# Performance work log

Hardware: AMD Instinct MI355X
Metric: run time of the kernel (lower is better)

## Reference

```python
import jax, jax.numpy as jnp
import numpy as np

SIG_EPS = 0.1
IN_DIM = 256
OUT_DIM = 64


def setup_inputs() -> dict:
    key = jax.random.key(0)
    ks = jax.random.split(key, 6)
    B, S, Q = 32, 512, 512
    return {
        "phi_support": jax.random.normal(ks[0], (B, S, IN_DIM), jnp.float32),
        "y_support": jax.random.normal(ks[1], (B, S, OUT_DIM), jnp.float32),
        "phi_query": jax.random.normal(ks[2], (B, Q, IN_DIM), jnp.float32),
        "y_query": jax.random.normal(ks[3], (B, Q, OUT_DIM), jnp.float32),
        # learned parameters (K init'd to zeros in torch, use small randn for a non-trivial test)
        "K": jax.random.normal(ks[4], (IN_DIM, OUT_DIM), jnp.float32) * 0.02,
        "L_asym": jax.random.normal(ks[5], (IN_DIM, IN_DIM), jnp.float32) * 0.1,
    }


def reference(phi_support, y_support, phi_query, y_query, K, L_asym):
    sig_eps = jnp.float32(SIG_EPS)
    log_sig_eps = jnp.log(sig_eps)
    out_dim = K.shape[1]

    L = L_asym @ L_asym.T  # [I, I]
    # nobs > 0 branch (n_support = 512)
    posterior_L = jnp.einsum('bsi,bsj->bij', phi_support, phi_support) + L[None]  # [B,I,I]
    posterior_L_inv = jnp.linalg.inv(posterior_L)
    rhs = jnp.einsum('bsi,bso->bio', phi_support, y_support) + (L @ K)[None]  # [B,I,O]
    posterior_K = posterior_L_inv @ rhs  # [B,I,O]

    mu_pred = phi_query @ posterior_K  # [B,Q,O]
    # spread_fac = 1 + diag quadratic form phi Linv phi^T  -> [B,Q]
    spread_fac = 1.0 + jnp.einsum('bqi,bij,bqj->bq', phi_query, posterior_L_inv, phi_query)
    eye_eps = jnp.eye(out_dim, dtype=phi_query.dtype) * sig_eps
    sig_pred = spread_fac[..., None, None] * eye_eps  # [B,Q,O,O]

    # predictive_nll: inverse of sig_pred is an exactly scaled identity, so the
    # quadratic form y^T inv(sig_pred) y == ||y||^2 / (spread_fac * sig_eps) (same math)
    diff = y_query - mu_pred
    quadf = jnp.sum(diff * diff, axis=-1) / (spread_fac * sig_eps)  # [B,Q]
    logdet = out_dim * (jnp.log(spread_fac) + log_sig_eps)  # [B,Q]
    predictive_nll = logdet.mean() + quadf.mean()

    return (mu_pred, sig_pred, predictive_nll)
```

## Files before the change

### kernel.cpp

```cpp
#include <hip/hip_runtime.h>
#include <math.h>

#define B 32
#define S 512
#define Q 512
#define I 256
#define O 64
#define SIG_EPS 0.1f
#define LOG_SIG_EPS (-2.3025850929940457f)

#define WS_L 0
#define WS_T1 (WS_L + 65536)
#define WS_LK (WS_T1 + 16384)
#define WS_M (WS_LK + 16384)
#define WS_RHS (WS_M + B * 65536)
#define WS_D (WS_RHS + B * 16384)
#define WS_PK (WS_D + 2 * B * 4096)
#define WS_SP (WS_PK + B * 16384)
#define WS_NLL (WS_SP + B * 512)

#define OUT_MU_ELEMS (B * Q * O)
#define OUT_SIG_ELEMS (B * Q * O * O)
#define OUT_NLL_IDX (OUT_MU_ELEMS + OUT_SIG_ELEMS)

__device__ __forceinline__ void fma4x4(const float4 av, const float4 bv, float acc[4][4]) {
  const float ar[4] = {av.x, av.y, av.z, av.w};
  const float br[4] = {bv.x, bv.y, bv.z, bv.w};
#pragma unroll
  for (int i = 0; i < 4; ++i)
#pragma unroll
    for (int j = 0; j < 4; ++j) acc[i][j] += ar[i] * br[j];
}

__device__ __forceinline__ void load_direct64(float* dst, int ds, const float* src, int ss, int t) {
#pragma unroll
  for (int m = 0; m < 4; ++m) {
    int r = (t >> 4) + 16 * m, c4 = (t & 15) * 4;
    *(float4*)&dst[r * ds + c4] = *(const float4*)&src[(size_t)r * ss + c4];
  }
}
__device__ __forceinline__ void load_trans64(float* dst, int ds , const float* src, int ss, int t) {
#pragma unroll
  for (int m = 0; m < 4; ++m) {
    int r = (t >> 4) + 16 * m, c4 = (t & 15) * 4;
    float4 v = *(const float4*)&src[(size_t)r * ss + c4];
    dst[(c4 + 0) * ds + r] = v.x;
    dst[(c4 + 1) * ds + r] = v.y;
    dst[(c4 + 2) * ds + r] = v.z;
    dst[(c4 + 3) * ds + r] = v.w;
  }
}
template <int SA, int SB>
__device__ __forceinline__ void gemm64(const float* At, const float* Bs, int tr, int tc, float acc[4][4]) {
#pragma unroll 8
  for (int kk = 0; kk < 64; ++kk) {
    float4 a = *(const float4*)&At[kk * SA + tr * 4];
    float4 b = *(const float4*)&Bs[kk * SB + tc * 4];
    fma4x4(a, b, acc);
  }
}

#define SC4(V) \
  V.x *= pivinv; V.y *= pivinv; V.z *= pivinv; V.w *= pivinv
#define UP4(V, R) \
  V.x -= g * R.x; V.y -= g * R.y; V.z -= g * R.z; V.w -= g * R.w

template <int TS>
__device__ void gj64(const float* T, float* rowbuf, float* Dout, int t) {
  int r = t >> 2, q = t & 3;
  int lane = t & 63;
  float4 A0 = *(const float4*)&T[r * TS + q * 16 + 0];
  float4 A1 = *(const float4*)&T[r * TS + q * 16 + 4];
  float4 A2 = *(const float4*)&T[r * TS + q * 16 + 8];
  float4 A3 = *(const float4*)&T[r * TS + q * 16 + 12];
#define IC(c) (((q * 16 + (c)) == r) ? 1.f : 0.f)
  float4 I0 = make_float4(IC(0), IC(1), IC(2), IC(3));
  float4 I1 = make_float4(IC(4), IC(5), IC(6), IC(7));
  float4 I2 = make_float4(IC(8), IC(9), IC(10), IC(11));
  float4 I3 = make_float4(IC(12), IC(13), IC(14), IC(15));
#undef IC
  for (int p = 0; p < 64; ++p) {
    float* RA = rowbuf + (p & 1) * 128;
    float* RI = RA + 64;
    if (r == p) {
      ((float4*)&RA[q * 16])[0] = A0; ((float4*)&RA[q * 16])[1] = A1;
      ((float4*)&RA[q * 16])[2] = A2; ((float4*)&RA[q * 16])[3] = A3;
      ((float4*)&RI[q * 16])[0] = I0; ((float4*)&RI[q * 16])[1] = I1;
      ((float4*)&RI[q * 16])[2] = I2; ((float4*)&RI[q * 16])[3] = I3;
    }
    __syncthreads();
    float pivinv = 1.0f / RA[p];
    int s = p & 15;
    float4 blk = (s < 8) ? ((s < 4) ? A0 : A1) : ((s < 12) ? A2 : A3);
    int sc = s & 3;
    float ap = (sc == 0) ? blk.x : (sc == 1) ? blk.y : (sc == 2) ? blk.z : blk.w;
    float f = __shfl(ap, (lane & ~3) | (p >> 4), 64);
    float4 ra0 = ((const float4*)&RA[q * 16])[0], ra1 = ((const float4*)&RA[q * 16])[1];
    float4 ra2 = ((const float4*)&RA[q * 16])[2], ra3 = ((const float4*)&RA[q * 16])[3];
    float4 ri0 = ((const float4*)&RI[q * 16])[0], ri1 = ((const float4*)&RI[q * 16])[1];
    float4 ri2 = ((const float4*)&RI[q * 16])[2], ri3 = ((const float4*)&RI[q * 16])[3];
    if (r == p) {
      SC4(A0); SC4(A1); SC4(A2); SC4(A3);
      SC4(I0); SC4(I1); SC4(I2); SC4(I3);
    } else {
      float g = f * pivinv;
      UP4(A0, ra0); UP4(A1, ra1); UP4(A2, ra2); UP4(A3, ra3);
      UP4(I0, ri0); UP4(I1, ri1); UP4(I2, ri2); UP4(I3, ri3);
    }
  }
  ((float4*)&Dout[r * 64 + q * 16])[0] = I0;
  ((float4*)&Dout[r * 64 + q * 16])[1] = I1;
  ((float4*)&Dout[r * 64 + q * 16])[2] = I2;
  ((float4*)&Dout[r * 64 + q * 16])[3] = I3;
}

__global__ __launch_bounds__(256) void k_pre1(const float* __restrict__ La, const float* __restrict__ Km,
                                              float* __restrict__ Lm, float* __restrict__ T1,
                                              float* __restrict__ spread, float* __restrict__ nllacc) {
  __shared__ float sA[16 * 68];
  __shared__ float sB[16 * 68];
  int blk = blockIdx.x, t = threadIdx.x;
  if (blk >= 20) {
    int idx = (blk - 20) * 256 + t;
    spread[idx] = 1.0f;
    if (idx == 0) nllacc[0] = 0.f;
    return;
  }
  int tr = t >> 4, tc = t & 15;
  float acc[4][4] = {};
  if (blk < 16) {
    int i0 = (blk >> 2) * 64, j0 = (blk & 3) * 64;
    for (int ks = 0; ks < 256; ks += 16) {
      __syncthreads();
#pragma unroll
      for (int m = 0; m < 4; ++m) {
        int r = (t >> 4) + 16 * m, kk = t & 15;
        sA[kk * 68 + r] = La[(size_t)(i0 + r) * 256 + ks + kk];
        sB[kk * 68 + r] = La[(size_t)(j0 + r) * 256 + ks + kk];
      }
      __syncthreads();
#pragma unroll
      for (int kk = 0; kk < 16; ++kk) {
        float4 a = *(const float4*)&sA[kk * 68 + tr * 4];
        float4 bv = *(const float4*)&sB[kk * 68 + tc * 4];
        fma4x4(a, bv, acc);
      }
    }
#pragma unroll
    for (int mi = 0; mi < 4; ++mi) {
      float4 v = {acc[mi][0], acc[mi][1], acc[mi][2], acc[mi][3]};
      *(float4*)&Lm[(size_t)(i0 + tr * 4 + mi) * 256 + j0 + tc * 4] = v;
    }
  } else {
    int i0 = (blk - 16) * 64;
    for (int ks = 0; ks < 256; ks += 16) {
      __syncthreads();
#pragma unroll
      for (int m = 0; m < 4; ++m) {
        int kk = (t >> 6) + 4 * m, c = t & 63;
        sA[kk * 68 + c] = La[(size_t)(ks + kk) * 256 + i0 + c];
        sB[kk * 68 + c] = Km[(size_t)(ks + kk) * 64 + c];
      }
      __syncthreads();
#pragma unroll
      for (int kk = 0; kk < 16; ++kk) {
        float4 a = *(const float4*)&sA[kk * 68 + tr * 4];
        float4 bv = *(const float4*)&sB[kk * 68 + tc * 4];
        fma4x4(a, bv, acc);
      }
    }
#pragma unroll
    for (int mi = 0; mi < 4; ++mi) {
      float4 v = {acc[mi][0], acc[mi][1], acc[mi][2], acc[mi][3]};
      *(float4*)&T1[(size_t)(i0 + tr * 4 + mi) * 64 + tc * 4] = v;
    }
  }
}

__global__ __launch_bounds__(256) void k_gram(const float* __restrict__ phi_s, const float* __restrict__ y_s,
                                              const float* __restrict__ Lm, const float* __restrict__ La,
                                              const float* __restrict__ T1, float* __restrict__ M,
                                              float* __restrict__ RHS, float* __restrict__ LK,
                                              float* __restrict__ Dbuf) {
  __shared__ float Ps[16][64];
  __shared__ float Ws[16][64];
  __shared__ float trbuf[64 * 68];
  __shared__ float rowbuf[256];
  int b = blockIdx.x, y = blockIdx.y;
  int t = threadIdx.x;
  int tr = t >> 4, tc = t & 15;
  float acc[4][4] = {};

  if (y == 14) {
    if (b >= 4) return;
    int i0 = b * 64;
    for (int ks = 0; ks < 256; ks += 16) {
      __syncthreads();
#pragma unroll
      for (int m = 0; m < 4; ++m) {
        trbuf[(t & 15) * 68 + (t >> 4) + 16 * m] = La[(size_t)(i0 + (t >> 4) + 16 * m) * 256 + ks + (t & 15)];
        Ws[(t >> 6) + 4 * m][t & 63] = T1[(size_t)(ks + (t >> 6) + 4 * m) * 64 + (t & 63)];
      }
      __syncthreads();
#pragma unroll
      for (int kk = 0; kk < 16; ++kk) {
        float4 a = *(const float4*)&trbuf[kk * 68 + tr * 4];
        float4 bv = *(const float4*)&Ws[kk][tc * 4];
        fma4x4(a, bv, acc);
      }
    }
#pragma unroll
    for (int mi = 0; mi < 4; ++mi) {
      float4 v = {acc[mi][0], acc[mi][1], acc[mi][2], acc[mi][3]};
      *(float4*)&LK[(size_t)(i0 + tr * 4 + mi) * 64 + tc * 4] = v;
    }
    return;
  }

  const int TI[10] = {0, 0, 0, 0, 1, 1, 1, 2, 2, 3};
  const int TJ[10] = {0, 1, 2, 3, 1, 2, 3, 2, 3, 3};
  bool isRHS = (y >= 10);
  int it = isRHS ? (y - 10) : TI[y];
  int jt = isRHS ? 0 : TJ[y];
  int i0 = it * 64, j0 = jt * 64;
  const float* Pb = phi_s + (size_t)b * S * I;
  const float* Wb = isRHS ? (y_s + (size_t)b * S * O) : Pb;
  int wstride = isRHS ? O : I;
  int wcol = isRHS ? 0 : j0;
  int lr = t >> 6, lc = t & 63;
  for (int ks = 0; ks < S; ks += 16) {
    __syncthreads();
#pragma unroll
    for (int m = 0; m < 4; ++m) {
      Ps[lr + 4 * m][lc] = Pb[(size_t)(ks + lr + 4 * m) * I + i0 + lc];
      Ws[lr + 4 * m][lc] = Wb[(size_t)(ks + lr + 4 * m) * wstride + wcol + lc];
    }
    __syncthreads();
#pragma unroll
    for (int kk = 0; kk < 16; ++kk) {
      float4 a = *(const float4*)&Ps[kk][tr * 4];
      float4 bv = *(const float4*)&Ws[kk][tc * 4];
      fma4x4(a, bv, acc);
    }
  }
  float* Mb = M + (size_t)b * 65536;
  if (!isRHS) {
#pragma unroll
    for (int mi = 0; mi < 4; ++mi) {
      int i = i0 + tr * 4 + mi;
      float4 add = *(const float4*)&Lm[(size_t)i * 256 + j0 + tc * 4];
      acc[mi][0] += add.x; acc[mi][1] += add.y; acc[mi][2] += add.z; acc[mi][3] += add.w;
      float4 v = {acc[mi][0], acc[mi][1], acc[mi][2], acc[mi][3]};
      *(float4*)&Mb[(size_t)i * 256 + j0 + tc * 4] = v;
    }
    if (it != jt) {
      __syncthreads();
#pragma unroll
      for (int mi = 0; mi < 4; ++mi)
#pragma unroll
        for (int cj = 0; cj < 4; ++cj) trbuf[(tc * 4 + cj) * 68 + tr * 4 + mi] = acc[mi][cj];
      __syncthreads();
#pragma unroll
      for (int m = 0; m < 4; ++m) {
        int rr = (t >> 4) + 16 * m, cc4 = (t & 15) * 4;
        float4 v = *(const float4*)&trbuf[rr * 68 + cc4];
        *(float4*)&Mb[(size_t)(j0 + rr) * 256 + i0 + cc4] = v;
      }
    } else if (it == 0) {
      __syncthreads();
#pragma unroll
      for (int mi = 0; mi < 4; ++mi) {
        float4 v = {acc[mi][0], acc[mi][1], acc[mi][2], acc[mi][3]};
        *(float4*)&trbuf[(tr * 4 + mi) * 68 + tc * 4] = v;
      }
      __syncthreads();
      gj64<68>(trbuf, rowbuf, Dbuf + (size_t)b * 4096, t);
    }
  } else {
#pragma unroll
    for (int mi = 0; mi < 4; ++mi) {
      float4 v = {acc[mi][0], acc[mi][1], acc[mi][2], acc[mi][3]};
      *(float4*)&RHS[(size_t)b * 16384 + (size_t)(i0 + tr * 4 + mi) * 64 + tc * 4] = v;
    }
  }
}

__global__ __launch_bounds__(256) void k_step(float* __restrict__ M, float* __restrict__ Dbuf, int kb) {
  __shared__ float shA[64 * 68];
  __shared__ float shB[64 * 64];
  __shared__ float shC[64 * 64];
  __shared__ float shD[64 * 68];
  __shared__ float rowbuf[256];
  int b = blockIdx.x, u = blockIdx.y;
  int i = u >> 2, j = u & 3;
  int t = threadIdx.x;
  int tr = t >> 4, tc = t & 15;
  float* Mb = M + (size_t)b * 65536;
  const float* Din = Dbuf + (size_t)(kb & 1) * (B * 4096) + (size_t)b * 4096;
  float* Dout = Dbuf + (size_t)((kb + 1) & 1) * (B * 4096) + (size_t)b * 4096;
  bool ik = (i == kb), jk = (j == kb);
  if (ik && jk) {
#pragma unroll
    for (int m = 0; m < 4; ++m) {
      int r = (t >> 4) + 16 * m, c4 = (t & 15) * 4;
      *(float4*)&Mb[(size_t)(kb * 64 + r) * 256 + kb * 64 + c4] = *(const float4*)&Din[r * 64 + c4];
    }
    return;
  }
  float acc[4][4] = {};
  if (ik) {
    load_trans64(shA, 68, Din, 64, t);
    load_direct64(shB, 64, &Mb[(size_t)(kb * 64) * 256 + j * 64], 256, t);
    __syncthreads();
    gemm64<68, 64>(shA, shB, tr, tc, acc);
#pragma unroll
    for (int mi = 0; mi < 4; ++mi) {
      float4 v = {acc[mi][0], acc[mi][1], acc[mi][2], acc[mi][3]};
      *(float4*)&Mb[(size_t)(kb * 64 + tr * 4 + mi) * 256 + j * 64 + tc * 4] = v;
    }
    return;
  }
  if (jk) {
    load_trans64(shA, 68, &Mb[(size_t)(i * 64) * 256 + kb * 64], 256, t);
    load_direct64(shB, 64, Din, 64, t);
    __syncthreads();
    gemm64<68, 64>(shA, shB, tr, tc, acc);
#pragma unroll
    for (int mi = 0; mi < 4; ++mi) {
      float4 v = {-acc[mi][0], -acc[mi][1], -acc[mi][2], -acc[mi][3]};
      *(float4*)&Mb[(size_t)(i * 64 + tr * 4 + mi) * 256 + kb * 64 + tc * 4] = v;
    }
    return;
  }
  load_trans64(shA, 68, Din, 64, t);
  load_direct64(shB, 64, &Mb[(size_t)(kb * 64) * 256 + j * 64], 256, t);
  load_trans64(shD, 68, &Mb[(size_t)(i * 64) * 256 + kb * 64], 256, t);
  __syncthreads();
  gemm64<68, 64>(shA, shB, tr, tc, acc);
#pragma unroll
  for (int mi = 0; mi < 4; ++mi) {
    float4 v = {acc[mi][0], acc[mi][1], acc[mi][2], acc[mi][3]};
    *(float4*)&shC[(tr * 4 + mi) * 64 + tc * 4] = v;
  }
  __syncthreads();
  float acc2[4][4] = {};
  gemm64<68, 64>(shD, shC, tr, tc, acc2);
  bool la = (kb < 3) && (i == kb + 1) && (j == kb + 1);
#pragma unroll
  for (int mi = 0; mi < 4; ++mi) {
    size_t off = (size_t)(i * 64 + tr * 4 + mi) * 256 + j * 64 + tc * 4;
    float4 old = *(const float4*)&Mb[off];
    float4 v = {old.x - acc2[mi][0], old.y - acc2[mi][1], old.z - acc2[mi][2], old.w - acc2[mi][3]};
    *(float4*)&Mb[off] = v;
    if (la) *(float4*)&shB[(tr * 4 + mi) * 64 + tc * 4] = v;
  }
  if (la) {
    __syncthreads();
    gj64<64>(shB, rowbuf, Dout, t);
  }
}

__global__ __launch_bounds__(256) void k_postK(const float* __restrict__ Minv, const float* __restrict__ RHS,
                                               const float* __restrict__ LK, float* __restrict__ PK) {
  int b = blockIdx.x, it = blockIdx.y;
  int i0 = it * 64;
  const float* A = Minv + (size_t)b * 65536;
  const float* G = RHS + (size_t)b * 16384;
  __shared__ float At[16][68];
  __shared__ float Bs[16][64];
  float acc[4][4] = {};
  int t = threadIdx.x, tr = t >> 4, tc = t & 15;
  int ar = t >> 2, ac4 = (t & 3) * 4;
  int br = t >> 6, bc = t & 63;
  for (int ks = 0; ks < 256; ks += 16) {
    __syncthreads();
    float4 av = *(const float4*)&A[(size_t)(i0 + ar) * 256 + ks + ac4];
    At[ac4 + 0][ar] = av.x; At[ac4 + 1][ar] = av.y; At[ac4 + 2][ar] = av.z; At[ac4 + 3][ar] = av.w;
#pragma unroll
    for (int m = 0; m < 4; ++m) {
      int kk = ks + br + 4 * m;
      Bs[br + 4 * m][bc] = G[(size_t)kk * 64 + bc] + LK[(size_t)kk * 64 + bc];
    }
    __syncthreads();
#pragma unroll
    for (int kk = 0; kk < 16; ++kk) {
      float4 a4 = *(const float4*)&At[kk][tr * 4];
      float4 b4 = *(const float4*)&Bs[kk][tc * 4];
      fma4x4(a4, b4, acc);
    }
  }
#pragma unroll
  for (int mi = 0; mi < 4; ++mi) {
    float4 v = {acc[mi][0], acc[mi][1], acc[mi][2], acc[mi][3]};
    *(float4*)&PK[(size_t)b * 16384 + (size_t)(i0 + tr * 4 + mi) * 64 + tc * 4] = v;
  }
}

__global__ __launch_bounds__(256) void k_muspread(const float* __restrict__ phi_q, const float* __restrict__ Minv,
                                                  const float* __restrict__ PK, float* __restrict__ mu,
                                                  float* __restrict__ spread) {
  int b = blockIdx.x, it = blockIdx.y, z = blockIdx.z;
  const float* A = phi_q + (size_t)b * Q * I;
  __shared__ float At[16][68];
  __shared__ float Bs[16][64];
  float acc[4][4] = {};
  int t = threadIdx.x, tr = t >> 4, tc = t & 15;
  int ar = t >> 2, ac4 = (t & 3) * 4;
  int br = t >> 6, bc = t & 63;
  int q0 = it * 64;
  if (z == 4) {
    const float* Bm = PK + (size_t)b * 16384;
    for (int ks = 0; ks < 256; ks += 16) {
      __syncthreads();
      float4 av = *(const float4*)&A[(size_t)(q0 + ar) * 256 + ks + ac4];
      At[ac4 + 0][ar] = av.x; At[ac4 + 1][ar] = av.y; At[ac4 + 2][ar] = av.z; At[ac4 + 3][ar] = av.w;
#pragma unroll
      for (int m = 0; m < 4; ++m) Bs[br + 4 * m][bc] = Bm[(size_t)(ks + br + 4 * m) * 64 + bc];
      __syncthreads();
#pragma unroll
      for (int kk = 0; kk < 16; ++kk) {
        float4 a4 = *(const float4*)&At[kk][tr * 4];
        float4 b4 = *(const float4*)&Bs[kk][tc * 4];
        fma4x4(a4, b4, acc);
      }
    }
#pragma unroll
    for (int mi = 0; mi < 4; ++mi) {
      float4 v = {acc[mi][0], acc[mi][1], acc[mi][2], acc[mi][3]};
      *(float4*)&mu[(size_t)b * Q * O + (size_t)(q0 + tr * 4 + mi) * 64 + tc * 4] = v;
    }
  } else {
    int j0 = z * 64;
    const float* Bm = Minv + (size_t)b * 65536;
    for (int ks = 0; ks < 256; ks += 16) {
      __syncthreads();
      float4 av = *(const float4*)&A[(size_t)(q0 + ar) * 256 + ks + ac4];
      At[ac4 + 0][ar] = av.x; At[ac4 + 1][ar] = av.y; At[ac4 + 2][ar] = av.z; At[ac4 + 3][ar] = av.w;
#pragma unroll
      for (int m = 0; m < 4; ++m) Bs[br + 4 * m][bc] = Bm[(size_t)(ks + br + 4 * m) * 256 + j0 + bc];
      __syncthreads();
#pragma unroll
      for (int kk = 0; kk < 16; ++kk) {
        float4 a4 = *(const float4*)&At[kk][tr * 4];
        float4 b4 = *(const float4*)&Bs[kk][tc * 4];
        fma4x4(a4, b4, acc);
      }
    }
    float rs[4];
#pragma unroll
    for (int mi = 0; mi < 4; ++mi) {
      int qrow = q0 + tr * 4 + mi;
      float4 pv = *(const float4*)&A[(size_t)qrow * 256 + j0 + tc * 4];
      rs[mi] = acc[mi][0] * pv.x + acc[mi][1] * pv.y + acc[mi][2] * pv.z + acc[mi][3] * pv.w;
    }
#pragma unroll
    for (int off = 1; off < 16; off <<= 1) {
#pragma unroll
      for (int mi = 0; mi < 4; ++mi) rs[mi] += __shfl_xor(rs[mi], off);
    }
    if (tc == 0) {
#pragma unroll
      for (int mi = 0; mi < 4; ++mi) atomicAdd(&spread[(size_t)b * Q + q0 + tr * 4 + mi], rs[mi]);
    }
  }
}

__global__ __launch_bounds__(256) void k_signll(const float* __restrict__ spread, float4* __restrict__ sig,
                                                const float* __restrict__ yq, const float* __restrict__ mu,
                                                float* __restrict__ nllacc) {
  int t = threadIdx.x;
  if (blockIdx.x < 65536) {
    size_t idx = (size_t)blockIdx.x * 256 + t;
    int p4 = (int)(idx & 15);
    int o = (int)((idx >> 4) & 63);
    size_t bq = idx >> 10;
    float sv = spread[bq] * SIG_EPS;
    float4 v;
    v.x = (p4 * 4 + 0 == o) ? sv : 0.f;
    v.y = (p4 * 4 + 1 == o) ? sv : 0.f;
    v.z = (p4 * 4 + 2 == o) ? sv : 0.f;
    v.w = (p4 * 4 + 3 == o) ? sv : 0.f;
    sig[idx] = v;
  } else {
    int bq = (blockIdx.x - 65536) * 256 + t;
    float sp = spread[bq];
    const float4* yv = (const float4*)(yq + (size_t)bq * 64);
    const float4* mv = (const float4*)(mu + (size_t)bq * 64);
    float ssd = 0.f;
#pragma unroll
    for (int i = 0; i < 16; ++i) {
      float4 a = yv[i], b = mv[i];
      float dx = a.x - b.x, dy = a.y - b.y, dz = a.z - b.z, dw = a.w - b.w;
      ssd += dx * dx + dy * dy + dz * dz + dw * dw;
    }
    float quadf = ssd / (sp * SIG_EPS);
    float ld = 64.0f * (logf(sp) + LOG_SIG_EPS);
    float val = (ld + quadf) * (1.0f / 16384.0f);
#pragma unroll
    for (int off = 32; off; off >>= 1) val += __shfl_down(val, off);
    if ((t & 63) == 0) atomicAdd(nllacc, val);
  }
}

__global__ void k_fin(const float* __restrict__ nllacc, float* __restrict__ out) {
  if (threadIdx.x == 0 && blockIdx.x == 0) out[0] = nllacc[0];
}

extern "C" void kernel_launch(void* const* d_in, const int* in_sizes, int n_in, void* d_out, int out_size,
                              void* d_ws, size_t ws_size, hipStream_t stream) {
  const float* phi_s = (const float*)d_in[0];
  const float* y_s = (const float*)d_in[1];
  const float* phi_q = (const float*)d_in[2];
  const float* y_q = (const float*)d_in[3];
  const float* Km = (const float*)d_in[4];
  const float* La = (const float*)d_in[5];

  float* ws = (float*)d_ws;
  float* Lm = ws + WS_L;
  float* T1 = ws + WS_T1;
  float* LKm = ws + WS_LK;
  float* Mbuf = ws + WS_M;
  float* RHSb = ws + WS_RHS;
  float* Dbuf = ws + WS_D;
  float* PKb = ws + WS_PK;
  float* spread = ws + WS_SP;
  float* nllacc = ws + WS_NLL;

  float* out_mu = (float*)d_out;
  float* out_sig = out_mu + OUT_MU_ELEMS;
  float* out_nll = out_mu + OUT_NLL_IDX;

  k_pre1<<<84, 256, 0, stream>>>(La, Km, Lm, T1, spread, nllacc);
  k_gram<<<dim3(B, 15), 256, 0, stream>>>(phi_s, y_s, Lm, La, T1, Mbuf, RHSb, LKm, Dbuf);
  for (int kb = 0; kb < 4; ++kb) k_step<<<dim3(B, 16), 256, 0, stream>>>(Mbuf, Dbuf, kb);
  k_postK<<<dim3(B, 4), 256, 0, stream>>>(Mbuf, RHSb, LKm, PKb);
  k_muspread<<<dim3(B, 8, 5), 256, 0, stream>>>(phi_q, Mbuf, PKb, out_mu, spread);
  k_signll<<<65600, 256, 0, stream>>>(spread, (float4*)out_sig, y_q, out_mu, nllacc);
  k_fin<<<1, 64, 0, stream>>>(nllacc, out_nll);
}
```

Before: 330.1 us.

## Move gram, posterior-K and mu/spread GEMMs to split-bf16 MFMA

Adds a conversion pass that writes phi_support and y_support as transposed hi/lo bf16 pairs. The Gram, RHS, posterior-K and mu/spread GEMMs now run on bf16 MFMA using three products (hh, hl, lh) to approximate fp32 accuracy. The blocked inversion now ping-pongs between two M buffers, and its final step emits the inverse directly as bf16 hi/lo. The spread atomics are replaced by a single direct write per query. The goal is to replace scalar fp32 FMA loops with matrix-core throughput, at the cost of extra conversion traffic, a larger workspace and a small precision risk. The 64M-element sig_pred write, which likely dominates, is unchanged.

```diff
diff --git a/kernel.cpp b/kernel.cpp
--- a/kernel.cpp
+++ b/kernel.cpp
@@ -10,19 +10,65 @@
 #define LOG_SIG_EPS (-2.3025850929940457f)
 
 #define WS_L 0
-#define WS_T1 (WS_L + 65536)
-#define WS_LK (WS_T1 + 16384)
-#define WS_M (WS_LK + 16384)
-#define WS_RHS (WS_M + B * 65536)
-#define WS_D (WS_RHS + B * 16384)
-#define WS_PK (WS_D + 2 * B * 4096)
-#define WS_SP (WS_PK + B * 16384)
-#define WS_NLL (WS_SP + B * 512)
+#define WS_T1 65536
+#define WS_LKT 81920
+#define WS_M0 98304
+#define WS_M1 2195456
+#define WS_RHST 4292608
+#define WS_D 4816896
+#define WS_SP 5079040
+#define WS_NLL 5095424
+#define WS_U16 5095488
+#define U_PTH 0
+#define U_PTL 4194304
+#define U_YTH 8388608
+#define U_YTL 9437184
+#define U_IVH 10485760
+#define U_IVL 12582912
+#define U_PKH 14680064
+#define U_PKL 15204352
 
 #define OUT_MU_ELEMS (B * Q * O)
 #define OUT_SIG_ELEMS (B * Q * O * O)
 #define OUT_NLL_IDX (OUT_MU_ELEMS + OUT_SIG_ELEMS)
 
+typedef short short8 __attribute__((ext_vector_type(8)));
+typedef float f32x4 __attribute__((ext_vector_type(4)));
+#define MFMA16(a, b, c) __builtin_amdgcn_mfma_f32_16x16x32_bf16(a, b, c, 0, 0, 0)
+
+__device__ __forceinline__ f32x4 mfma3(short8 ah, short8 al, short8 bh, short8 bl, f32x4 c) {
+  c = MFMA16(ah, bh, c);
+  c = MFMA16(ah, bl, c);
+  c = MFMA16(al, bh, c);
+  return c;
+}
+
+__device__ __forceinline__ unsigned short f2bf(float x) {
+  unsigned int u = __float_as_uint(x);
+  return (unsigned short)((u + 0x7fffu + ((u >> 16) & 1u)) >> 16);
+}
+__device__ __forceinline__ float bf2f(unsigned short h) { return __uint_as_float(((unsigned int)h) << 16); }
+__device__ __forceinline__ void split2(float x, unsigned short& h, unsigned short& l) {
+  h = f2bf(x);
+  l = f2bf(x - bf2f(h));
+}
+__device__ __forceinline__ void split4(float4 v, uint2& H, uint2& L) {
+  unsigned short h0, h1, h2, h3, l0, l1, l2, l3;
+  split2(v.x, h0, l0); split2(v.y, h1, l1); split2(v.z, h2, l2); split2(v.w, h3, l3);
+  H.x = (unsigned)h0 | ((unsigned)h1 << 16); H.y = (unsigned)h2 | ((unsigned)h3 << 16);
+  L.x = (unsigned)l0 | ((unsigned)l1 << 16); L.y = (unsigned)l2 | ((unsigned)l3 << 16);
+}
+__device__ __forceinline__ void cvt8(const float* p, short8& h8, short8& l8) {
+  float4 a = *(const float4*)p;
+  float4 b = *(const float4*)(p + 4);
+  uint2 H0, L0, H1, L1;
+  split4(a, H0, L0); split4(b, H1, L1);
+  union { uint2 q[2]; short8 s; } uh, ul;
+  uh.q[0] = H0; uh.q[1] = H1; ul.q[0] = L0; ul.q[1] = L1;
+  h8 = uh.s; l8 = ul.s;
+}
+__device__ __forceinline__ short8 ld8(const unsigned short* p) { return *(const short8*)(const void*)p; }
+
 __device__ __forceinline__ void fma4x4(const float4 av, const float4 bv, float acc[4][4]) {
   const float ar[4] = {av.x, av.y, av.z, av.w};
   const float br[4] = {bv.x, bv.y, bv.z, bv.w};
@@ -39,7 +85,7 @@
     *(float4*)&dst[r * ds + c4] = *(const float4*)&src[(size_t)r * ss + c4];
   }
 }
-__device__ __forceinline__ void load_trans64(float* dst, int ds , const float* src, int ss, int t) {
+__device__ __forceinline__ void load_trans64(float* dst, int ds, const float* src, int ss, int t) {
 #pragma unroll
   for (int m = 0; m < 4; ++m) {
     int r = (t >> 4) + 16 * m, c4 = (t & 15) * 4;
@@ -60,10 +106,8 @@
   }
 }
 
-#define SC4(V) \
-  V.x *= pivinv; V.y *= pivinv; V.z *= pivinv; V.w *= pivinv
-#define UP4(V, R) \
-  V.x -= g * R.x; V.y -= g * R.y; V.z -= g * R.z; V.w -= g * R.w
+#define SC4(V) V.x *= pivinv; V.y *= pivinv; V.z *= pivinv; V.w *= pivinv
+#define UP4(V, R) V.x -= g * R.x; V.y -= g * R.y; V.z -= g * R.z; V.w -= g * R.w
 
 template <int TS>
 __device__ void gj64(const float* T, float* rowbuf, float* Dout, int t) {
@@ -114,18 +158,60 @@
   ((float4*)&Dout[r * 64 + q * 16])[3] = I3;
 }
 
+__global__ __launch_bounds__(256) void k_cvt(const float* __restrict__ phi_s, const float* __restrict__ y_s,
+                                             unsigned short* __restrict__ PTh, unsigned short* __restrict__ PTl,
+                                             unsigned short* __restrict__ YTh, unsigned short* __restrict__ YTl,
+                                             float* __restrict__ nllacc) {
+  __shared__ unsigned short Hs[64][68];
+  __shared__ unsigned short Lo[64][68];
+  int blk = blockIdx.x, t = threadIdx.x;
+  if (blk == 0 && t == 0) nllacc[0] = 0.f;
+  const float* src;
+  unsigned short *dh, *dl;
+  int sstride;
+  if (blk < 1024) {
+    int b = blk >> 5, r = blk & 31, ic = r >> 3, sc = r & 7;
+    src = phi_s + ((size_t)b * 512 + sc * 64) * 256 + ic * 64;
+    sstride = 256;
+    size_t d0 = ((size_t)b * 256 + ic * 64) * 512 + sc * 64;
+    dh = PTh + d0; dl = PTl + d0;
+  } else {
+    int qq = blk - 1024, b = qq >> 3, sc = qq & 7;
+    src = y_s + ((size_t)b * 512 + sc * 64) * 64;
+    sstride = 64;
+    size_t d0 = ((size_t)b * 64) * 512 + sc * 64;
+    dh = YTh + d0; dl = YTl + d0;
+  }
+  int c = t & 63, rb = (t >> 6) * 16;
+#pragma unroll
+  for (int m = 0; m < 16; ++m) {
+    int s = rb + m;
+    float x = src[(size_t)s * sstride + c];
+    unsigned short h, l;
+    split2(x, h, l);
+    Hs[c][s] = h;
+    Lo[c][s] = l;
+  }
+  __syncthreads();
+  int il0 = t >> 4, c4 = (t & 15) * 4;
+#pragma unroll
+  for (int m = 0; m < 4; ++m) {
+    int il = il0 + 16 * m;
+    uint2 H, L;
+    H.x = (unsigned)Hs[il][c4] | ((unsigned)Hs[il][c4 + 1] << 16);
+    H.y = (unsigned)Hs[il][c4 + 2] | ((unsigned)Hs[il][c4 + 3] << 16);
+    L.x = (unsigned)Lo[il][c4] | ((unsigned)Lo[il][c4 + 1] << 16);
+    L.y = (unsigned)Lo[il][c4 + 2] | ((unsigned)Lo[il][c4 + 3] << 16);
+    *(uint2*)&dh[(size_t)il * 512 + c4] = H;
+    *(uint2*)&dl[(size_t)il * 512 + c4] = L;
+  }
+}
+
 __global__ __launch_bounds__(256) void k_pre1(const float* __restrict__ La, const float* __restrict__ Km,
-                                              float* __restrict__ Lm, float* __restrict__ T1,
-                                              float* __restrict__ spread, float* __restrict__ nllacc) {
+                                              float* __restrict__ Lm, float* __restrict__ T1) {
   __shared__ float sA[16 * 68];
   __shared__ float sB[16 * 68];
   int blk = blockIdx.x, t = threadIdx.x;
-  if (blk >= 20) {
-    int idx = (blk - 20) * 256 + t;
-    spread[idx] = 1.0f;
-    if (idx == 0) nllacc[0] = 0.f;
-    return;
-  }
   int tr = t >> 4, tc = t & 15;
   float acc[4][4] = {};
   if (blk < 16) {
@@ -177,115 +263,132 @@
   }
 }
 
-__global__ __launch_bounds__(256) void k_gram(const float* __restrict__ phi_s, const float* __restrict__ y_s,
-                                              const float* __restrict__ Lm, const float* __restrict__ La,
-                                              const float* __restrict__ T1, float* __restrict__ M,
-                                              float* __restrict__ RHS, float* __restrict__ LK,
-                                              float* __restrict__ Dbuf) {
-  __shared__ float Ps[16][64];
-  __shared__ float Ws[16][64];
+__global__ __launch_bounds__(256) void k_gram(
+    const unsigned short* __restrict__ PTh, const unsigned short* __restrict__ PTl,
+    const unsigned short* __restrict__ YTh, const unsigned short* __restrict__ YTl,
+    const float* __restrict__ Lm, const float* __restrict__ La, const float* __restrict__ T1,
+    float* __restrict__ M0, float* __restrict__ RHST, float* __restrict__ LKT, float* __restrict__ Dbuf) {
   __shared__ float trbuf[64 * 68];
   __shared__ float rowbuf[256];
-  int b = blockIdx.x, y = blockIdx.y;
-  int t = threadIdx.x;
-  int tr = t >> 4, tc = t & 15;
-  float acc[4][4] = {};
+  __shared__ float Ws[16 * 64];
+  int b = blockIdx.x, y = blockIdx.y, t = threadIdx.x;
 
   if (y == 14) {
     if (b >= 4) return;
     int i0 = b * 64;
+    int tr = t >> 4, tc = t & 15;
+    float acc[4][4] = {};
     for (int ks = 0; ks < 256; ks += 16) {
       __syncthreads();
 #pragma unroll
       for (int m = 0; m < 4; ++m) {
         trbuf[(t & 15) * 68 + (t >> 4) + 16 * m] = La[(size_t)(i0 + (t >> 4) + 16 * m) * 256 + ks + (t & 15)];
-        Ws[(t >> 6) + 4 * m][t & 63] = T1[(size_t)(ks + (t >> 6) + 4 * m) * 64 + (t & 63)];
+        Ws[((t >> 6) + 4 * m) * 64 + (t & 63)] = T1[(size_t)(ks + (t >> 6) + 4 * m) * 64 + (t & 63)];
       }
       __syncthreads();
 #pragma unroll
       for (int kk = 0; kk < 16; ++kk) {
         float4 a = *(const float4*)&trbuf[kk * 68 + tr * 4];
-        float4 bv = *(const float4*)&Ws[kk][tc * 4];
+        float4 bv = *(const float4*)&Ws[kk * 64 + tc * 4];
         fma4x4(a, bv, acc);
       }
     }
-#pragma unroll
-    for (int mi = 0; mi < 4; ++mi) {
-      float4 v = {acc[mi][0], acc[mi][1], acc[mi][2], acc[mi][3]};
-      *(float4*)&LK[(size_t)(i0 + tr * 4 + mi) * 64 + tc * 4] = v;
+    __syncthreads();
+#pragma unroll
+    for (int mi = 0; mi < 4; ++mi)
+#pragma unroll
+      for (int cj = 0; cj < 4; ++cj) trbuf[(tr * 4 + mi) * 68 + tc * 4 + cj] = acc[mi][cj];
+    __syncthreads();
+    int rr0 = t >> 4, cc4 = (t & 15) * 4;
+#pragma unroll
+    for (int m = 0; m < 4; ++m) {
+      int rr = rr0 + 16 * m;
+      float4 v = {trbuf[(cc4 + 0) * 68 + rr], trbuf[(cc4 + 1) * 68 + rr], trbuf[(cc4 + 2) * 68 + rr],
+                  trbuf[(cc4 + 3) * 68 + rr]};
+      *(float4*)&LKT[(size_t)rr * 256 + i0 + cc4] = v;
     }
     return;
   }
 
-  const int TI[10] = {0, 0, 0, 0, 1, 1, 1, 2, 2, 3};
-  const int TJ[10] = {0, 1, 2, 3, 1, 2, 3, 2, 3, 3};
-  bool isRHS = (y >= 10);
-  int it = isRHS ? (y - 10) : TI[y];
-  int jt = isRHS ? 0 : TJ[y];
-  int i0 = it * 64, j0 = jt * 64;
-  const float* Pb = phi_s + (size_t)b * S * I;
-  const float* Wb = isRHS ? (y_s + (size_t)b * S * O) : Pb;
-  int wstride = isRHS ? O : I;
-  int wcol = isRHS ? 0 : j0;
-  int lr = t >> 6, lc = t & 63;
-  for (int ks = 0; ks < S; ks += 16) {
-    __syncthreads();
+  const int TIa[14] = {0, 0, 0, 0, 1, 1, 1, 2, 2, 3, 0, 1, 2, 3};
+  const int TJa[14] = {0, 1, 2, 3, 1, 2, 3, 2, 3, 3, 0, 0, 0, 0};
+  bool isR = (y >= 10);
+  int it = TIa[y], jt = TJa[y];
+  int i0 = it * 64, j0 = isR ? 0 : jt * 64;
+  int lane = t & 63, w = t >> 6, wr = w >> 1, wc = w & 1;
+  const unsigned short* Ah = PTh + (size_t)b * 256 * 512;
+  const unsigned short* Al = PTl + (size_t)b * 256 * 512;
+  const unsigned short* Bh = isR ? (YTh + (size_t)b * 64 * 512) : Ah;
+  const unsigned short* Bl = isR ? (YTl + (size_t)b * 64 * 512) : Al;
+  int ra0 = i0 + wr * 32 + (lane & 15);
+  int rb0 = j0 + wc * 32 + (lane & 15);
+  int klane = (lane >> 4) * 8;
+  f32x4 acc[2][2] = {};
+  for (int ks = 0; ks < 512; ks += 32) {
+    int kk = ks + klane;
+    short8 a0h = ld8(Ah + (size_t)ra0 * 512 + kk);
+    short8 a1h = ld8(Ah + (size_t)(ra0 + 16) * 512 + kk);
+    short8 a0l = ld8(Al + (size_t)ra0 * 512 + kk);
+    short8 a1l = ld8(Al + (size_t)(ra0 + 16) * 512 + kk);
+    short8 b0h = ld8(Bh + (size_t)rb0 * 512 + kk);
+    short8 b1h = ld8(Bh + (size_t)(rb0 + 16) * 512 + kk);
+    short8 b0l = ld8(Bl + (size_t)rb0 * 512 + kk);
+    short8 b1l = ld8(Bl + (size_t)(rb0 + 16) * 512 + kk);
+    acc[0][0] = mfma3(a0h, a0l, b0h, b0l, acc[0][0]);
+    acc[0][1] = mfma3(a0h, a0l, b1h, b1l, acc[0][1]);
+    acc[1][0] = mfma3(a1h, a1l, b0h, b0l, acc[1][0]);
+    acc[1][1] = mfma3(a1h, a1l, b1h, b1l, acc[1][1]);
+  }
+#pragma unroll
+  for (int ti = 0; ti < 2; ++ti)
+#pragma unroll
+    for (int tj = 0; tj < 2; ++tj)
+#pragma unroll
+      for (int r = 0; r < 4; ++r)
+        trbuf[(wr * 32 + ti * 16 + (lane >> 4) * 4 + r) * 68 + wc * 32 + tj * 16 + (lane & 15)] = acc[ti][tj][r];
+  __syncthreads();
+  int rr0 = t >> 4, cc4 = (t & 15) * 4;
+  if (!isR) {
+    float* Mb = M0 + (size_t)b * 65536;
+    bool d00 = (it == 0 && jt == 0);
 #pragma unroll
     for (int m = 0; m < 4; ++m) {
-      Ps[lr + 4 * m][lc] = Pb[(size_t)(ks + lr + 4 * m) * I + i0 + lc];
-      Ws[lr + 4 * m][lc] = Wb[(size_t)(ks + lr + 4 * m) * wstride + wcol + lc];
-    }
-    __syncthreads();
-#pragma unroll
-    for (int kk = 0; kk < 16; ++kk) {
-      float4 a = *(const float4*)&Ps[kk][tr * 4];
-      float4 bv = *(const float4*)&Ws[kk][tc * 4];
-      fma4x4(a, bv, acc);
-    }
-  }
-  float* Mb = M + (size_t)b * 65536;
-  if (!isRHS) {
-#pragma unroll
-    for (int mi = 0; mi < 4; ++mi) {
-      int i = i0 + tr * 4 + mi;
-      float4 add = *(const float4*)&Lm[(size_t)i * 256 + j0 + tc * 4];
-      acc[mi][0] += add.x; acc[mi][1] += add.y; acc[mi][2] += add.z; acc[mi][3] += add.w;
-      float4 v = {acc[mi][0], acc[mi][1], acc[mi][2], acc[mi][3]};
-      *(float4*)&Mb[(size_t)i * 256 + j0 + tc * 4] = v;
+      int rr = rr0 + 16 * m;
+      float4 v = *(float4*)&trbuf[rr * 68 + cc4];
+      float4 lv = *(const float4*)&Lm[(size_t)(i0 + rr) * 256 + j0 + cc4];
+      v.x += lv.x; v.y += lv.y; v.z += lv.z; v.w += lv.w;
+      *(float4*)&Mb[(size_t)(i0 + rr) * 256 + j0 + cc4] = v;
+      if (d00) *(float4*)&trbuf[rr * 68 + cc4] = v;
     }
     if (it != jt) {
-      __syncthreads();
-#pragma unroll
-      for (int mi = 0; mi < 4; ++mi)
-#pragma unroll
-        for (int cj = 0; cj < 4; ++cj) trbuf[(tc * 4 + cj) * 68 + tr * 4 + mi] = acc[mi][cj];
-      __syncthreads();
 #pragma unroll
       for (int m = 0; m < 4; ++m) {
-        int rr = (t >> 4) + 16 * m, cc4 = (t & 15) * 4;
-        float4 v = *(const float4*)&trbuf[rr * 68 + cc4];
+        int rr = rr0 + 16 * m;
+        float4 v = {trbuf[(cc4 + 0) * 68 + rr], trbuf[(cc4 + 1) * 68 + rr], trbuf[(cc4 + 2) * 68 + rr],
+                    trbuf[(cc4 + 3) * 68 + rr]};
+        float4 lv = *(const float4*)&Lm[(size_t)(j0 + rr) * 256 + i0 + cc4];
+        v.x += lv.x; v.y += lv.y; v.z += lv.z; v.w += lv.w;
         *(float4*)&Mb[(size_t)(j0 + rr) * 256 + i0 + cc4] = v;
       }
-    } else if (it == 0) {
-      __syncthreads();
-#pragma unroll
-      for (int mi = 0; mi < 4; ++mi) {
-        float4 v = {acc[mi][0], acc[mi][1], acc[mi][2], acc[mi][3]};
-        *(float4*)&trbuf[(tr * 4 + mi) * 68 + tc * 4] = v;
-      }
+    }
+    if (d00) {
       __syncthreads();
       gj64<68>(trbuf, rowbuf, Dbuf + (size_t)b * 4096, t);
     }
   } else {
 #pragma unroll
-    for (int mi = 0; mi < 4; ++mi) {
-      float4 v = {acc[mi][0], acc[mi][1], acc[mi][2], acc[mi][3]};
-      *(float4*)&RHS[(size_t)b * 16384 + (size_t)(i0 + tr * 4 + mi) * 64 + tc * 4] = v;
-    }
-  }
-}
-
-__global__ __launch_bounds__(256) void k_step(float* __restrict__ M, float* __restrict__ Dbuf, int kb) {
+    for (int m = 0; m < 4; ++m) {
+      int rr = rr0 + 16 * m;
+      float4 v = {trbuf[(cc4 + 0) * 68 + rr], trbuf[(cc4 + 1) * 68 + rr], trbuf[(cc4 + 2) * 68 + rr],
+                  trbuf[(cc4 + 3) * 68 + rr]};
+      *(float4*)&RHST[((size_t)b * 64 + rr) * 256 + i0 + cc4] = v;
+    }
+  }
+}
+
+__global__ __launch_bounds__(256) void k_step(const float* __restrict__ Msrc_, float* __restrict__ Mdst_,
+                                              float* __restrict__ Dbuf, unsigned short* __restrict__ IVh,
+                                              unsigned short* __restrict__ IVl, int kb) {
   __shared__ float shA[64 * 68];
   __shared__ float shB[64 * 64];
   __shared__ float shC[64 * 64];
@@ -295,46 +398,60 @@
   int i = u >> 2, j = u & 3;
   int t = threadIdx.x;
   int tr = t >> 4, tc = t & 15;
-  float* Mb = M + (size_t)b * 65536;
+  const float* Ms = Msrc_ + (size_t)b * 65536;
+  float* Md = Mdst_ + (size_t)b * 65536;
   const float* Din = Dbuf + (size_t)(kb & 1) * (B * 4096) + (size_t)b * 4096;
   float* Dout = Dbuf + (size_t)((kb + 1) & 1) * (B * 4096) + (size_t)b * 4096;
+  bool last = (kb == 3);
+  unsigned short* Yh = IVh + (size_t)b * 65536;
+  unsigned short* Yl = IVl + (size_t)b * 65536;
+  auto STORE = [&](int row, int col, float4 v) {
+    if (last) {
+      uint2 H, L;
+      split4(v, H, L);
+      *(uint2*)&Yh[(size_t)row * 256 + col] = H;
+      *(uint2*)&Yl[(size_t)row * 256 + col] = L;
+    } else {
+      *(float4*)&Md[(size_t)row * 256 + col] = v;
+    }
+  };
   bool ik = (i == kb), jk = (j == kb);
   if (ik && jk) {
 #pragma unroll
     for (int m = 0; m < 4; ++m) {
       int r = (t >> 4) + 16 * m, c4 = (t & 15) * 4;
-      *(float4*)&Mb[(size_t)(kb * 64 + r) * 256 + kb * 64 + c4] = *(const float4*)&Din[r * 64 + c4];
+      STORE(kb * 64 + r, kb * 64 + c4, *(const float4*)&Din[r * 64 + c4]);
     }
     return;
   }
   float acc[4][4] = {};
   if (ik) {
     load_trans64(shA, 68, Din, 64, t);
-    load_direct64(shB, 64, &Mb[(size_t)(kb * 64) * 256 + j * 64], 256, t);
+    load_direct64(shB, 64, &Ms[(size_t)(kb * 64) * 256 + j * 64], 256, t);
     __syncthreads();
     gemm64<68, 64>(shA, shB, tr, tc, acc);
 #pragma unroll
     for (int mi = 0; mi < 4; ++mi) {
       float4 v = {acc[mi][0], acc[mi][1], acc[mi][2], acc[mi][3]};
-      *(float4*)&Mb[(size_t)(kb * 64 + tr * 4 + mi) * 256 + j * 64 + tc * 4] = v;
+      STORE(kb * 64 + tr * 4 + mi, j * 64 + tc * 4, v);
     }
     return;
   }
   if (jk) {
-    load_trans64(shA, 68, &Mb[(size_t)(i * 64) * 256 + kb * 64], 256, t);
+    load_trans64(shA, 68, &Ms[(size_t)(i * 64) * 256 + kb * 64], 256, t);
     load_direct64(shB, 64, Din, 64, t);
     __syncthreads();
     gemm64<68, 64>(shA, shB, tr, tc, acc);
 #pragma unroll
     for (int mi = 0; mi < 4; ++mi) {
       float4 v = {-acc[mi][0], -acc[mi][1], -acc[mi][2], -acc[mi][3]};
-      *(float4*)&Mb[(size_t)(i * 64 + tr * 4 + mi) * 256 + kb * 64 + tc * 4] = v;
+      STORE(i * 64 + tr * 4 + mi, kb * 64 + tc * 4, v);
     }
     return;
   }
   load_trans64(shA, 68, Din, 64, t);
-  load_direct64(shB, 64, &Mb[(size_t)(kb * 64) * 256 + j * 64], 256, t);
-  load_trans64(shD, 68, &Mb[(size_t)(i * 64) * 256 + kb * 64], 256, t);
+  load_direct64(shB, 64, &Ms[(size_t)(kb * 64) * 256 + j * 64], 256, t);
+  load_trans64(shD, 68, &Ms[(size_t)(i * 64) * 256 + kb * 64], 256, t);
   __syncthreads();
   gemm64<68, 64>(shA, shB, tr, tc, acc);
 #pragma unroll
@@ -349,9 +466,9 @@
 #pragma unroll
   for (int mi = 0; mi < 4; ++mi) {
     size_t off = (size_t)(i * 64 + tr * 4 + mi) * 256 + j * 64 + tc * 4;
-    float4 old = *(const float4*)&Mb[off];
+    float4 old = *(const float4*)&Ms[off];
     float4 v = {old.x - acc2[mi][0], old.y - acc2[mi][1], old.z - acc2[mi][2], old.w - acc2[mi][3]};
-    *(float4*)&Mb[off] = v;
+    STORE(i * 64 + tr * 4 + mi, j * 64 + tc * 4, v);
     if (la) *(float4*)&shB[(tr * 4 + mi) * 64 + tc * 4] = v;
   }
   if (la) {
@@ -360,108 +477,112 @@
   }
 }
 
-__global__ __launch_bounds__(256) void k_postK(const float* __restrict__ Minv, const float* __restrict__ RHS,
-                                               const float* __restrict__ LK, float* __restrict__ PK) {
-  int b = blockIdx.x, it = blockIdx.y;
-  int i0 = it * 64;
-  const float* A = Minv + (size_t)b * 65536;
-  const float* G = RHS + (size_t)b * 16384;
-  __shared__ float At[16][68];
-  __shared__ float Bs[16][64];
-  float acc[4][4] = {};
-  int t = threadIdx.x, tr = t >> 4, tc = t & 15;
-  int ar = t >> 2, ac4 = (t & 3) * 4;
-  int br = t >> 6, bc = t & 63;
-  for (int ks = 0; ks < 256; ks += 16) {
-    __syncthreads();
-    float4 av = *(const float4*)&A[(size_t)(i0 + ar) * 256 + ks + ac4];
-    At[ac4 + 0][ar] = av.x; At[ac4 + 1][ar] = av.y; At[ac4 + 2][ar] = av.z; At[ac4 + 3][ar] = av.w;
-#pragma unroll
-    for (int m = 0; m < 4; ++m) {
-      int kk = ks + br + 4 * m;
-      Bs[br + 4 * m][bc] = G[(size_t)kk * 64 + bc] + LK[(size_t)kk * 64 + bc];
-    }
-    __syncthreads();
-#pragma unroll
-    for (int kk = 0; kk < 16; ++kk) {
-      float4 a4 = *(const float4*)&At[kk][tr * 4];
-      float4 b4 = *(const float4*)&Bs[kk][tc * 4];
-      fma4x4(a4, b4, acc);
-    }
-  }
-#pragma unroll
-  for (int mi = 0; mi < 4; ++mi) {
-    float4 v = {acc[mi][0], acc[mi][1], acc[mi][2], acc[mi][3]};
-    *(float4*)&PK[(size_t)b * 16384 + (size_t)(i0 + tr * 4 + mi) * 64 + tc * 4] = v;
-  }
-}
-
-__global__ __launch_bounds__(256) void k_muspread(const float* __restrict__ phi_q, const float* __restrict__ Minv,
-                                                  const float* __restrict__ PK, float* __restrict__ mu,
-                                                  float* __restrict__ spread) {
-  int b = blockIdx.x, it = blockIdx.y, z = blockIdx.z;
-  const float* A = phi_q + (size_t)b * Q * I;
-  __shared__ float At[16][68];
-  __shared__ float Bs[16][64];
-  float acc[4][4] = {};
-  int t = threadIdx.x, tr = t >> 4, tc = t & 15;
-  int ar = t >> 2, ac4 = (t & 3) * 4;
-  int br = t >> 6, bc = t & 63;
-  int q0 = it * 64;
-  if (z == 4) {
-    const float* Bm = PK + (size_t)b * 16384;
-    for (int ks = 0; ks < 256; ks += 16) {
-      __syncthreads();
-      float4 av = *(const float4*)&A[(size_t)(q0 + ar) * 256 + ks + ac4];
-      At[ac4 + 0][ar] = av.x; At[ac4 + 1][ar] = av.y; At[ac4 + 2][ar] = av.z; At[ac4 + 3][ar] = av.w;
-#pragma unroll
-      for (int m = 0; m < 4; ++m) Bs[br + 4 * m][bc] = Bm[(size_t)(ks + br + 4 * m) * 64 + bc];
-      __syncthreads();
-#pragma unroll
-      for (int kk = 0; kk < 16; ++kk) {
-        float4 a4 = *(const float4*)&At[kk][tr * 4];
-        float4 b4 = *(const float4*)&Bs[kk][tc * 4];
-        fma4x4(a4, b4, acc);
-      }
-    }
-#pragma unroll
-    for (int mi = 0; mi < 4; ++mi) {
-      float4 v = {acc[mi][0], acc[mi][1], acc[mi][2], acc[mi][3]};
-      *(float4*)&mu[(size_t)b * Q * O + (size_t)(q0 + tr * 4 + mi) * 64 + tc * 4] = v;
-    }
-  } else {
-    int j0 = z * 64;
-    const float* Bm = Minv + (size_t)b * 65536;
-    for (int ks = 0; ks < 256; ks += 16) {
-      __syncthreads();
-      float4 av = *(const float4*)&A[(size_t)(q0 + ar) * 256 + ks + ac4];
-      At[ac4 + 0][ar] = av.x; At[ac4 + 1][ar] = av.y; At[ac4 + 2][ar] = av.z; At[ac4 + 3][ar] = av.w;
-#pragma unroll
-      for (int m = 0; m < 4; ++m) Bs[br + 4 * m][bc] = Bm[(size_t)(ks + br + 4 * m) * 256 + j0 + bc];
-      __syncthreads();
-#pragma unroll
-      for (int kk = 0; kk < 16; ++kk) {
-        float4 a4 = *(const float4*)&At[kk][tr * 4];
-        float4 b4 = *(const float4*)&Bs[kk][tc * 4];
-        fma4x4(a4, b4, acc);
-      }
-    }
-    float rs[4];
-#pragma unroll
-    for (int mi = 0; mi < 4; ++mi) {
-      int qrow = q0 + tr * 4 + mi;
-      float4 pv = *(const float4*)&A[(size_t)qrow * 256 + j0 + tc * 4];
-      rs[mi] = acc[mi][0] * pv.x + acc[mi][1] * pv.y + acc[mi][2] * pv.z + acc[mi][3] * pv.w;
-    }
-#pragma unroll
-    for (int off = 1; off < 16; off <<= 1) {
-#pragma unroll
-      for (int mi = 0; mi < 4; ++mi) rs[mi] += __shfl_xor(rs[mi], off);
-    }
-    if (tc == 0) {
-#pragma unroll
-      for (int mi = 0; mi < 4; ++mi) atomicAdd(&spread[(size_t)b * Q + q0 + tr * 4 + mi], rs[mi]);
-    }
+__global__ __launch_bounds__(256) void k_postK(const unsigned short* __restrict__ IVh,
+                                               const unsigned short* __restrict__ IVl,
+                                               const float* __restrict__ RHST, const float* __restrict__ LKT,
+                                               unsigned short* __restrict__ PKh, unsigned short* __restrict__ PKl) {
+  int b = blockIdx.x, i0 = blockIdx.y * 64, t = threadIdx.x;
+  int lane = t & 63, w = t >> 6, wr = w >> 1, wc = w & 1;
+  const unsigned short* Ah = IVh + (size_t)b * 65536;
+  const unsigned short* Al = IVl + (size_t)b * 65536;
+  int ra0 = i0 + wr * 32 + (lane & 15);
+  int ob0 = wc * 32 + (lane & 15);
+  int klane = (lane >> 4) * 8;
+  f32x4 acc[2][2] = {};
+  for (int ks = 0; ks < 256; ks += 32) {
+    int kk = ks + klane;
+    short8 a0h = ld8(Ah + (size_t)ra0 * 256 + kk);
+    short8 a1h = ld8(Ah + (size_t)(ra0 + 16) * 256 + kk);
+    short8 a0l = ld8(Al + (size_t)ra0 * 256 + kk);
+    short8 a1l = ld8(Al + (size_t)(ra0 + 16) * 256 + kk);
+    short8 bh[2], bl[2];
+#pragma unroll
+    for (int s = 0; s < 2; ++s) {
+      int o = ob0 + s * 16;
+      float g[8];
+      float4 g0 = *(const float4*)&RHST[((size_t)b * 64 + o) * 256 + kk];
+      float4 g1 = *(const float4*)&RHST[((size_t)b * 64 + o) * 256 + kk + 4];
+      float4 l0 = *(const float4*)&LKT[(size_t)o * 256 + kk];
+      float4 l1 = *(const float4*)&LKT[(size_t)o * 256 + kk + 4];
+      g[0] = g0.x + l0.x; g[1] = g0.y + l0.y; g[2] = g0.z + l0.z; g[3] = g0.w + l0.w;
+      g[4] = g1.x + l1.x; g[5] = g1.y + l1.y; g[6] = g1.z + l1.z; g[7] = g1.w + l1.w;
+      cvt8(g, bh[s], bl[s]);
+    }
+    acc[0][0] = mfma3(a0h, a0l, bh[0], bl[0], acc[0][0]);
+    acc[0][1] = mfma3(a0h, a0l, bh[1], bl[1], acc[0][1]);
+    acc[1][0] = mfma3(a1h, a1l, bh[0], bl[0], acc[1][0]);
+    acc[1][1] = mfma3(a1h, a1l, bh[1], bl[1], acc[1][1]);
+  }
+#pragma unroll
+  for (int ti = 0; ti < 2; ++ti)
+#pragma unroll
+    for (int tj = 0; tj < 2; ++tj) {
+      int ib = i0 + wr * 32 + ti * 16 + (lane >> 4) * 4;
+      int o = wc * 32 + tj * 16 + (lane & 15);
+      float4 v = {acc[ti][tj][0], acc[ti][tj][1], acc[ti][tj][2], acc[ti][tj][3]};
+      uint2 H, L;
+      split4(v, H, L);
+      *(uint2*)&PKh[((size_t)b * 64 + o) * 256 + ib] = H;
+      *(uint2*)&PKl[((size_t)b * 64 + o) * 256 + ib] = L;
+    }
+}
+
+__global__ __launch_bounds__(256) void k_musp(const float* __restrict__ phi_q,
+                                              const unsigned short* __restrict__ IVh,
+                                              const unsigned short* __restrict__ IVl,
+                                              const unsigned short* __restrict__ PKh,
+                                              const unsigned short* __restrict__ PKl, float* __restrict__ mu,
+                                              float* __restrict__ spread) {
+  int b = blockIdx.x, qb = blockIdx.y * 64, t = threadIdx.x;
+  int lane = t & 63, w = t >> 6;
+  int qs = qb + w * 16;
+  int qlane = qs + (lane & 15);
+  int klane = (lane >> 4) * 8;
+  const float* Pq = phi_q + (size_t)b * 512 * 256;
+  short8 ah[8], al[8];
+#pragma unroll
+  for (int k8 = 0; k8 < 8; ++k8) cvt8(&Pq[(size_t)qlane * 256 + k8 * 32 + klane], ah[k8], al[k8]);
+  const unsigned short* Kh = PKh + (size_t)b * 64 * 256;
+  const unsigned short* Kl = PKl + (size_t)b * 64 * 256;
+#pragma unroll
+  for (int ot = 0; ot < 4; ++ot) {
+    f32x4 acc = {};
+    int orow = ot * 16 + (lane & 15);
+#pragma unroll
+    for (int k8 = 0; k8 < 8; ++k8) {
+      short8 bh = ld8(Kh + (size_t)orow * 256 + k8 * 32 + klane);
+      short8 bl = ld8(Kl + (size_t)orow * 256 + k8 * 32 + klane);
+      acc = mfma3(ah[k8], al[k8], bh, bl, acc);
+    }
+#pragma unroll
+    for (int r = 0; r < 4; ++r)
+      mu[((size_t)b * 512 + qs + (lane >> 4) * 4 + r) * 64 + ot * 16 + (lane & 15)] = acc[r];
+  }
+  const unsigned short* Vh = IVh + (size_t)b * 65536;
+  const unsigned short* Vl = IVl + (size_t)b * 65536;
+  float rs[4] = {0.f, 0.f, 0.f, 0.f};
+  for (int jt = 0; jt < 16; ++jt) {
+    f32x4 acc = {};
+    int jrow = jt * 16 + (lane & 15);
+#pragma unroll
+    for (int k8 = 0; k8 < 8; ++k8) {
+      short8 bh = ld8(Vh + (size_t)jrow * 256 + k8 * 32 + klane);
+      short8 bl = ld8(Vl + (size_t)jrow * 256 + k8 * 32 + klane);
+      acc = mfma3(ah[k8], al[k8], bh, bl, acc);
+    }
+#pragma unroll
+    for (int r = 0; r < 4; ++r) {
+      int q = qs + (lane >> 4) * 4 + r;
+      rs[r] += acc[r] * Pq[(size_t)q * 256 + jt * 16 + (lane & 15)];
+    }
+  }
+#pragma unroll
+  for (int off = 1; off < 16; off <<= 1)
+#pragma unroll
+    for (int r = 0; r < 4; ++r) rs[r] += __shfl_xor(rs[r], off);
+  if ((lane & 15) == 0) {
+#pragma unroll
+    for (int r = 0; r < 4; ++r) spread[(size_t)b * 512 + qs + (lane >> 4) * 4 + r] = 1.0f + rs[r];
   }
 }
 
@@ -518,23 +639,36 @@
   float* ws = (float*)d_ws;
   float* Lm = ws + WS_L;
   float* T1 = ws + WS_T1;
-  float* LKm = ws + WS_LK;
-  float* Mbuf = ws + WS_M;
-  float* RHSb = ws + WS_RHS;
+  float* LKT = ws + WS_LKT;
+  float* M0 = ws + WS_M0;
+  float* M1 = ws + WS_M1;
+  float* RHST = ws + WS_RHST;
   float* Dbuf = ws + WS_D;
-  float* PKb = ws + WS_PK;
   float* spread = ws + WS_SP;
   float* nllacc = ws + WS_NLL;
+  unsigned short* u16b = (unsigned short*)(ws + WS_U16);
+  unsigned short* PTh = u16b + U_PTH;
+  unsigned short* PTl = u16b + U_PTL;
+  unsigned short* YTh = u16b + U_YTH;
+  unsigned short* YTl = u16b + U_YTL;
+  unsigned short* IVh = u16b + U_IVH;
+  unsigned short* IVl = u16b + U_IVL;
+  unsigned short* PKh = u16b + U_PKH;
+  unsigned short* PKl = u16b + U_PKL;
 
   float* out_mu = (float*)d_out;
   float* out_sig = out_mu + OUT_MU_ELEMS;
   float* out_nll = out_mu + OUT_NLL_IDX;
 
-  k_pre1<<<84, 256, 0, stream>>>(La, Km, Lm, T1, spread, nllacc);
-  k_gram<<<dim3(B, 15), 256, 0, stream>>>(phi_s, y_s, Lm, La, T1, Mbuf, RHSb, LKm, Dbuf);
-  for (int kb = 0; kb < 4; ++kb) k_step<<<dim3(B, 16), 256, 0, stream>>>(Mbuf, Dbuf, kb);
-  k_postK<<<dim3(B, 4), 256, 0, stream>>>(Mbuf, RHSb, LKm, PKb);
-  k_muspread<<<dim3(B, 8, 5), 256, 0, stream>>>(phi_q, Mbuf, PKb, out_mu, spread);
+  k_cvt<<<1280, 256, 0, stream>>>(phi_s, y_s, PTh, PTl, YTh, YTl, nllacc);
+  k_pre1<<<20, 256, 0, stream>>>(La, Km, Lm, T1);
+  k_gram<<<dim3(B, 15), 256, 0, stream>>>(PTh, PTl, YTh, YTl, Lm, La, T1, M0, RHST, LKT, Dbuf);
+  k_step<<<dim3(B, 16), 256, 0, stream>>>(M0, M1, Dbuf, IVh, IVl, 0);
+  k_step<<<dim3(B, 16), 256, 0, stream>>>(M1, M0, Dbuf, IVh, IVl, 1);
+  k_step<<<dim3(B, 16), 256, 0, stream>>>(M0, M1, Dbuf, IVh, IVl, 2);
+  k_step<<<dim3(B, 16), 256, 0, stream>>>(M1, M0, Dbuf, IVh, IVl, 3);
+  k_postK<<<dim3(B, 4), 256, 0, stream>>>(IVh, IVl, RHST, LKT, PKh, PKl);
+  k_musp<<<dim3(B, 8), 256, 0, stream>>>(phi_q, IVh, IVl, PKh, PKl, out_mu, spread);
   k_signll<<<65600, 256, 0, stream>>>(spread, (float4*)out_sig, y_q, out_mu, nllacc);
   k_fin<<<1, 64, 0, stream>>>(nllacc, out_nll);
 }
```

Result: no change. 336.0 us (+1.8%).
